# Kernel tuning notes

Hardware: AMD Instinct MI355X
Metric: run time of the kernel (lower is better)

Reference implementation:

```python
import jax, jax.numpy as jnp
import numpy as np

N_NODES = 100000
D_FEAT = 128            # per-embedding width; concat of 4 -> 512
INPUT_DIM = 4 * D_FEAT
HIDDEN_DIM = 64
N_SAMPLES = 250000


def _glorot(key, fan_in, fan_out):
    r = np.sqrt(6.0 / fan_in).astype(np.float32)
    return jax.random.uniform(key, (fan_in, fan_out), minval=-r, maxval=r, dtype=jnp.float32)


def setup_inputs() -> dict:
    key = jax.random.key(0)
    k1, k2, k3, k4, k5 = jax.random.split(key, 5)
    input1 = jax.random.normal(k1, (N_NODES, D_FEAT), dtype=jnp.float32)
    input2 = jax.random.normal(k2, (N_NODES, D_FEAT), dtype=jnp.float32)
    train_sample = jax.random.randint(k3, (N_SAMPLES, 2), 0, N_NODES, dtype=jnp.int64)
    w1 = _glorot(k4, INPUT_DIM, HIDDEN_DIM)
    b1 = jnp.zeros((HIDDEN_DIM,), dtype=jnp.float32)
    w2 = _glorot(k5, HIDDEN_DIM, 1)
    return {"input1": input1, "input2": input2, "train_sample": train_sample,
            "w1": w1, "b1": b1, "w2": w2}


def reference(input1, input2, train_sample, w1, b1, w2):
    src = train_sample[:, 0]
    dst = train_sample[:, 1]
    # four gathers + concat -> [E, 4*D_FEAT]
    h = jnp.concatenate([input1[src], input1[dst], input2[src], input2[dst]], axis=1)
    x = jax.nn.relu(h @ w1 + b1)          # [E, HIDDEN_DIM]
    return x @ w2                          # [E, 1]
```

## Files before the change

kernel.cpp:

```cpp
#include <hip/hip_runtime.h>
#include <hip/hip_bf16.h>

#define NN  100000
#define DF  128
#define HD  64
#define NS  250000


typedef __attribute__((ext_vector_type(8))) short bfrag;
typedef __attribute__((ext_vector_type(4))) float ffrag;

__device__ __forceinline__ unsigned short bf16bits(float f) {
    __hip_bfloat16 b = __float2bfloat16(f);
    return *(unsigned short*)&b;
}
__device__ __forceinline__ unsigned pack2(float a, float b) {
    return (unsigned)bf16bits(a) | ((unsigned)bf16bits(b) << 16);
}

__global__ __launch_bounds__(256) void prep_w1_kernel(
    const float* __restrict__ w1, unsigned short* __restrict__ Bf)
{
    const int gid  = blockIdx.x * 256 + threadIdx.x;
    const int lane = gid & 63;
    const int ks   = (gid >> 6) & 3;
    const int tn   = (gid >> 8) & 7;
    const int T    = gid >> 11;

    const int n     = tn * 16 + (lane & 15);
    const int kbase = ks * 32 + (lane >> 4) * 8;
    const int row0  = T * 256 + ((n >= 64) ? 128 : 0);
    const int col   = n & 63;

    float v[8];
    #pragma unroll
    for (int j = 0; j < 8; ++j) v[j] = w1[(size_t)(row0 + kbase + j) * HD + col];

    uint4 u;
    u.x = pack2(v[0], v[1]); u.y = pack2(v[2], v[3]);
    u.z = pack2(v[4], v[5]); u.w = pack2(v[6], v[7]);
    *(uint4*)(Bf + (size_t)gid * 8) = u;
}

__global__ __launch_bounds__(256) void node_gemm_mfma(
    const float* __restrict__ in1,
    const float* __restrict__ in2,
    const unsigned short* __restrict__ Bf,
    float* __restrict__ P)
{
    __shared__ unsigned short albs[2048];

    const int t  = threadIdx.x;
    const int T  = (blockIdx.x >= NN / 16) ? 1 : 0;
    const int m0 = (blockIdx.x - T * (NN / 16)) * 16;
    const float* in = T ? in2 : in1;

    {
        const int r    = t >> 4;
        const int qq   = t & 15;
        const int ks   = qq >> 2;
        const int quad = qq & 3;
        const int la   = quad * 16 + r;
        const float* src = in + (size_t)(m0 + r) * DF + qq * 8;
        const float4 f0 = *(const float4*)(src);
        const float4 f1 = *(const float4*)(src + 4);
        uint4 u;
        u.x = pack2(f0.x, f0.y); u.y = pack2(f0.z, f0.w);
        u.z = pack2(f1.x, f1.y); u.w = pack2(f1.z, f1.w);
        *(uint4*)(&albs[ks * 512 + la * 8]) = u;
    }
    __syncthreads();

    const int lane = t & 63;
    const int w    = t >> 6;

    bfrag bf[2][4];
    #pragma unroll
    for (int ti = 0; ti < 2; ++ti) {
        const int tn = w * 2 + ti;
        #pragma unroll
        for (int ks = 0; ks < 4; ++ks) {
            const size_t off = ((((size_t)T * 8 + tn) * 4 + ks) * 64 + lane) * 8;
            bf[ti][ks] = *(const bfrag*)(Bf + off);
        }
    }

    bfrag af[4];
    #pragma unroll
    for (int ks = 0; ks < 4; ++ks)
        af[ks] = *(const bfrag*)(&albs[ks * 512 + lane * 8]);

    ffrag acc[2] = {{0.f, 0.f, 0.f, 0.f}, {0.f, 0.f, 0.f, 0.f}};
    #pragma unroll
    for (int ks = 0; ks < 4; ++ks) {
        acc[0] = __builtin_amdgcn_mfma_f32_16x16x32_bf16(af[ks], bf[0][ks], acc[0], 0, 0, 0);
        acc[1] = __builtin_amdgcn_mfma_f32_16x16x32_bf16(af[ks], bf[1][ks], acc[1], 0, 0, 0);
    }

    const int col = lane & 15;
    const int rq  = lane >> 4;
    float* Pb = P + (size_t)T * NN * 128 + (size_t)m0 * 128;
    #pragma unroll
    for (int ti = 0; ti < 2; ++ti) {
        const int nb = (w * 2 + ti) * 16 + col;
        #pragma unroll
        for (int reg = 0; reg < 4; ++reg)
            Pb[(size_t)(rq * 4 + reg) * 128 + nb] = acc[ti][reg];
    }
}

__global__ __launch_bounds__(256) void edge_mlp_kernel(
    const float* __restrict__ P,
    const int*   __restrict__ ts,
    const float* __restrict__ b1,
    const float* __restrict__ w2,
    float* __restrict__ out)
{
    const int t = threadIdx.x;
    const int s = blockIdx.x * 16 + (t >> 4);
    const int l = t & 15;
    const int j = l * 4;

    const int2 e = ((const int2*)ts)[s];
    const float* Pa = P;
    const float* Pbt = P + (size_t)NN * 128;

    const float4 a0 = *(const float4*)(Pa  + (size_t)e.x * 128 + j);
    const float4 a1 = *(const float4*)(Pa  + (size_t)e.y * 128 + 64 + j);
    const float4 c0 = *(const float4*)(Pbt + (size_t)e.x * 128 + j);
    const float4 c1 = *(const float4*)(Pbt + (size_t)e.y * 128 + 64 + j);
    const float4 bb = *(const float4*)(b1 + j);
    const float4 ww = *(const float4*)(w2 + j);

    float p = 0.f;
    float x;
    x = a0.x + a1.x + c0.x + c1.x + bb.x; x = x > 0.f ? x : 0.f; p += x * ww.x;
    x = a0.y + a1.y + c0.y + c1.y + bb.y; x = x > 0.f ? x : 0.f; p += x * ww.y;
    x = a0.z + a1.z + c0.z + c1.z + bb.z; x = x > 0.f ? x : 0.f; p += x * ww.z;
    x = a0.w + a1.w + c0.w + c1.w + bb.w; x = x > 0.f ? x : 0.f; p += x * ww.w;

    p += __shfl_xor(p, 1);
    p += __shfl_xor(p, 2);
    p += __shfl_xor(p, 4);
    p += __shfl_xor(p, 8);
    if (l == 0) out[s] = p;
}

extern "C" void kernel_launch(void* const* d_in, const int* in_sizes, int n_in,
                              void* d_out, int out_size, void* d_ws, size_t ws_size,
                              hipStream_t stream) {
    const float* in1 = (const float*)d_in[0];
    const float* in2 = (const float*)d_in[1];
    const int*   ts  = (const int*)  d_in[2];
    const float* w1  = (const float*)d_in[3];
    const float* b1  = (const float*)d_in[4];
    const float* w2  = (const float*)d_in[5];
    float* out = (float*)d_out;

    float* P = (float*)d_ws;
    const size_t Pbytes = (size_t)2 * NN * 128 * sizeof(float);
    unsigned short* Bf;
    if (ws_size >= Pbytes + 65536)
        Bf = (unsigned short*)((char*)d_ws + Pbytes);
    else
        Bf = (unsigned short*)d_out;

    prep_w1_kernel<<<16, 256, 0, stream>>>(w1, Bf);
    node_gemm_mfma<<<2 * (NN / 16), 256, 0, stream>>>(in1, in2, Bf, P);
    edge_mlp_kernel<<<NS / 16, 256, 0, stream>>>(P, ts, b1, w2, out);
}
```

Measured before the change: 181.2 us.

## Fuse both node tables into one K=256 GEMM and store projections as bf16

The node GEMM now concatenates in1 and in2 rows along K (256), so each node yields one combined 128-wide projection in place of two separate tables that were summed per edge. The projection buffer is stored in bf16 through an LDS-staged coalesced write, which halves its footprint. The edge kernel then gathers two 8-byte chunks per lane instead of four 16-byte chunks. The trade-off is extra rounding from storing the pre-activation partial sums in bf16.

```diff
diff --git a/kernel.cpp b/kernel.cpp
--- a/kernel.cpp
+++ b/kernel.cpp
@@ -17,28 +17,39 @@
 __device__ __forceinline__ unsigned pack2(float a, float b) {
     return (unsigned)bf16bits(a) | ((unsigned)bf16bits(b) << 16);
 }
+__device__ __forceinline__ float bflo(unsigned u) {
+    union { unsigned i; float f; } c; c.i = u << 16; return c.f;
+}
+__device__ __forceinline__ float bfhi(unsigned u) {
+    union { unsigned i; float f; } c; c.i = u & 0xffff0000u; return c.f;
+}
 
 __global__ __launch_bounds__(256) void prep_w1_kernel(
     const float* __restrict__ w1, unsigned short* __restrict__ Bf)
 {
     const int gid  = blockIdx.x * 256 + threadIdx.x;
     const int lane = gid & 63;
-    const int ks   = (gid >> 6) & 3;
-    const int tn   = (gid >> 8) & 7;
-    const int T    = gid >> 11;
+    const int ks   = (gid >> 6) & 7;
+    const int tn   = gid >> 9;
 
     const int n     = tn * 16 + (lane & 15);
     const int kbase = ks * 32 + (lane >> 4) * 8;
-    const int row0  = T * 256 + ((n >= 64) ? 128 : 0);
     const int col   = n & 63;
 
-    float v[8];
+    uint4 u;
+    unsigned p[4];
     #pragma unroll
-    for (int j = 0; j < 8; ++j) v[j] = w1[(size_t)(row0 + kbase + j) * HD + col];
-
-    uint4 u;
-    u.x = pack2(v[0], v[1]); u.y = pack2(v[2], v[3]);
-    u.z = pack2(v[4], v[5]); u.w = pack2(v[6], v[7]);
+    for (int jp = 0; jp < 4; ++jp) {
+        float v[2];
+        #pragma unroll
+        for (int h = 0; h < 2; ++h) {
+            const int k = kbase + jp * 2 + h;
+            const int row = ((k >= 128) ? 256 : 0) + ((n >= 64) ? 128 : 0) + (k & 127);
+            v[h] = w1[(size_t)row * HD + col];
+        }
+        p[jp] = pack2(v[0], v[1]);
+    }
+    u.x = p[0]; u.y = p[1]; u.z = p[2]; u.w = p[3];
     *(uint4*)(Bf + (size_t)gid * 8) = u;
 }
 
@@ -46,71 +57,81 @@
     const float* __restrict__ in1,
     const float* __restrict__ in2,
     const unsigned short* __restrict__ Bf,
-    float* __restrict__ P)
+    unsigned short* __restrict__ Pn)
 {
-    __shared__ unsigned short albs[2048];
+    __shared__ unsigned short smem[4096];
 
     const int t  = threadIdx.x;
-    const int T  = (blockIdx.x >= NN / 16) ? 1 : 0;
-    const int m0 = (blockIdx.x - T * (NN / 16)) * 16;
-    const float* in = T ? in2 : in1;
+    const int m0 = blockIdx.x * 16;
 
     {
-        const int r    = t >> 4;
-        const int qq   = t & 15;
-        const int ks   = qq >> 2;
-        const int quad = qq & 3;
-        const int la   = quad * 16 + r;
-        const float* src = in + (size_t)(m0 + r) * DF + qq * 8;
+        const int r  = t >> 4;
+        const int qq = t & 15;
+        const float* src = (qq < 8)
+            ? in1 + (size_t)(m0 + r) * DF + qq * 16
+            : in2 + (size_t)(m0 + r) * DF + (qq - 8) * 16;
         const float4 f0 = *(const float4*)(src);
         const float4 f1 = *(const float4*)(src + 4);
-        uint4 u;
-        u.x = pack2(f0.x, f0.y); u.y = pack2(f0.z, f0.w);
-        u.z = pack2(f1.x, f1.y); u.w = pack2(f1.z, f1.w);
-        *(uint4*)(&albs[ks * 512 + la * 8]) = u;
+        const float4 f2 = *(const float4*)(src + 8);
+        const float4 f3 = *(const float4*)(src + 12);
+        uint4 u0, u1;
+        u0.x = pack2(f0.x, f0.y); u0.y = pack2(f0.z, f0.w);
+        u0.z = pack2(f1.x, f1.y); u0.w = pack2(f1.z, f1.w);
+        u1.x = pack2(f2.x, f2.y); u1.y = pack2(f2.z, f2.w);
+        u1.z = pack2(f3.x, f3.y); u1.w = pack2(f3.z, f3.w);
+        const int g0 = qq * 2, g1 = qq * 2 + 1;
+        *(uint4*)(&smem[(g0 >> 2) * 512 + ((g0 & 3) * 16 + r) * 8]) = u0;
+        *(uint4*)(&smem[(g1 >> 2) * 512 + ((g1 & 3) * 16 + r) * 8]) = u1;
     }
     __syncthreads();
 
     const int lane = t & 63;
     const int w    = t >> 6;
 
-    bfrag bf[2][4];
+    bfrag bf[2][8];
     #pragma unroll
     for (int ti = 0; ti < 2; ++ti) {
         const int tn = w * 2 + ti;
         #pragma unroll
-        for (int ks = 0; ks < 4; ++ks) {
-            const size_t off = ((((size_t)T * 8 + tn) * 4 + ks) * 64 + lane) * 8;
-            bf[ti][ks] = *(const bfrag*)(Bf + off);
-        }
+        for (int ks = 0; ks < 8; ++ks)
+            bf[ti][ks] = *(const bfrag*)(Bf + ((size_t)(tn * 8 + ks) * 64 + lane) * 8);
     }
 
-    bfrag af[4];
+    bfrag af[8];
     #pragma unroll
-    for (int ks = 0; ks < 4; ++ks)
-        af[ks] = *(const bfrag*)(&albs[ks * 512 + lane * 8]);
+    for (int ks = 0; ks < 8; ++ks)
+        af[ks] = *(const bfrag*)(&smem[ks * 512 + lane * 8]);
 
     ffrag acc[2] = {{0.f, 0.f, 0.f, 0.f}, {0.f, 0.f, 0.f, 0.f}};
     #pragma unroll
-    for (int ks = 0; ks < 4; ++ks) {
+    for (int ks = 0; ks < 8; ++ks) {
         acc[0] = __builtin_amdgcn_mfma_f32_16x16x32_bf16(af[ks], bf[0][ks], acc[0], 0, 0, 0);
         acc[1] = __builtin_amdgcn_mfma_f32_16x16x32_bf16(af[ks], bf[1][ks], acc[1], 0, 0, 0);
     }
 
-    const int col = lane & 15;
-    const int rq  = lane >> 4;
-    float* Pb = P + (size_t)T * NN * 128 + (size_t)m0 * 128;
-    #pragma unroll
-    for (int ti = 0; ti < 2; ++ti) {
-        const int nb = (w * 2 + ti) * 16 + col;
+    __syncthreads();
+    {
+        const int col = lane & 15;
+        const int rq  = lane >> 4;
         #pragma unroll
-        for (int reg = 0; reg < 4; ++reg)
-            Pb[(size_t)(rq * 4 + reg) * 128 + nb] = acc[ti][reg];
+        for (int ti = 0; ti < 2; ++ti) {
+            const int nc = (w * 2 + ti) * 16 + col;
+            #pragma unroll
+            for (int reg = 0; reg < 4; ++reg)
+                smem[(rq * 4 + reg) * 128 + nc] = bf16bits(acc[ti][reg]);
+        }
+    }
+    __syncthreads();
+    {
+        const int row = t >> 4;
+        const int seg = t & 15;
+        const uint4 u = *(const uint4*)(&smem[row * 128 + seg * 8]);
+        *(uint4*)(Pn + (size_t)(m0 + row) * 128 + seg * 8) = u;
     }
 }
 
 __global__ __launch_bounds__(256) void edge_mlp_kernel(
-    const float* __restrict__ P,
+    const unsigned short* __restrict__ Pn,
     const int*   __restrict__ ts,
     const float* __restrict__ b1,
     const float* __restrict__ w2,
@@ -122,22 +143,16 @@
     const int j = l * 4;
 
     const int2 e = ((const int2*)ts)[s];
-    const float* Pa = P;
-    const float* Pbt = P + (size_t)NN * 128;
-
-    const float4 a0 = *(const float4*)(Pa  + (size_t)e.x * 128 + j);
-    const float4 a1 = *(const float4*)(Pa  + (size_t)e.y * 128 + 64 + j);
-    const float4 c0 = *(const float4*)(Pbt + (size_t)e.x * 128 + j);
-    const float4 c1 = *(const float4*)(Pbt + (size_t)e.y * 128 + 64 + j);
+    const uint2 uu = *(const uint2*)(Pn + (size_t)e.x * 128 + j);
+    const uint2 vv = *(const uint2*)(Pn + (size_t)e.y * 128 + 64 + j);
     const float4 bb = *(const float4*)(b1 + j);
     const float4 ww = *(const float4*)(w2 + j);
 
-    float p = 0.f;
-    float x;
-    x = a0.x + a1.x + c0.x + c1.x + bb.x; x = x > 0.f ? x : 0.f; p += x * ww.x;
-    x = a0.y + a1.y + c0.y + c1.y + bb.y; x = x > 0.f ? x : 0.f; p += x * ww.y;
-    x = a0.z + a1.z + c0.z + c1.z + bb.z; x = x > 0.f ? x : 0.f; p += x * ww.z;
-    x = a0.w + a1.w + c0.w + c1.w + bb.w; x = x > 0.f ? x : 0.f; p += x * ww.w;
+    float p = 0.f, x;
+    x = bflo(uu.x) + bflo(vv.x) + bb.x; x = x > 0.f ? x : 0.f; p += x * ww.x;
+    x = bfhi(uu.x) + bfhi(vv.x) + bb.y; x = x > 0.f ? x : 0.f; p += x * ww.y;
+    x = bflo(uu.y) + bflo(vv.y) + bb.z; x = x > 0.f ? x : 0.f; p += x * ww.z;
+    x = bfhi(uu.y) + bfhi(vv.y) + bb.w; x = x > 0.f ? x : 0.f; p += x * ww.w;
 
     p += __shfl_xor(p, 1);
     p += __shfl_xor(p, 2);
@@ -157,8 +172,8 @@
     const float* w2  = (const float*)d_in[5];
     float* out = (float*)d_out;
 
-    float* P = (float*)d_ws;
-    const size_t Pbytes = (size_t)2 * NN * 128 * sizeof(float);
+    unsigned short* Pn = (unsigned short*)d_ws;
+    const size_t Pbytes = (size_t)NN * 128 * sizeof(unsigned short);
     unsigned short* Bf;
     if (ws_size >= Pbytes + 65536)
         Bf = (unsigned short*)((char*)d_ws + Pbytes);
@@ -166,6 +181,6 @@
         Bf = (unsigned short*)d_out;
 
     prep_w1_kernel<<<16, 256, 0, stream>>>(w1, Bf);
-    node_gemm_mfma<<<2 * (NN / 16), 256, 0, stream>>>(in1, in2, Bf, P);
-    edge_mlp_kernel<<<NS / 16, 256, 0, stream>>>(P, ts, b1, w2, out);
+    node_gemm_mfma<<<NN / 16, 256, 0, stream>>>(in1, in2, Bf, Pn);
+    edge_mlp_kernel<<<NS / 16, 256, 0, stream>>>(Pn, ts, b1, w2, out);
 }
```

After: 158.7 us. -12.4%, faster.
